# Performance work log

Hardware: AMD Instinct MI355X
Metric: run time of the kernel (lower is better)

Reference implementation:

```python
import jax, jax.numpy as jnp
import numpy as np

B, N_FRAMES, C, S = 4, 32, 256, 16
D = 512            # attn_dim = min(C*S*S, 512)
NHEADS = 8
TOKEN = C * S * S  # 65536
EPS = 1e-5


def _layer_norm_last(x, g, b):
    mu = x.mean(-1, keepdims=True)
    var = x.var(-1, keepdims=True)
    return (x - mu) * jax.lax.rsqrt(var + EPS) * g + b


def _forward(feat, Wp, bp, Wu, bu, Wq, bq, Wk, bk, Wv, bv, Wo, bo, ln1_g, ln1_b,
             Wk1, bk1, Wk2, bk2, Wpc, bpc, gn_g, gn_b, Wf1, bf1, Wf2, bf2,
             dn_g, dn_b, num_frames):
    BN, Cc, H, W = feat.shape
    N = num_frames
    Bb = BN // N
    # 1) flatten frames to tokens and project (B, N, token_dim) -> (B, N, D)
    tokens = feat.reshape(Bb, N, Cc * H * W)
    tp = tokens @ Wp.T + bp
    # contextual grouping with clamped indices: K = v_{n-1}, Q = v_n, V = v_{n+1}
    idx = jnp.arange(N)
    v_prev = tp[:, jnp.maximum(idx - 1, 0)]
    v_next = tp[:, jnp.minimum(idx + 1, N - 1)]
    # 2) MHA with seq_len 1 for Q/K/V (degenerate softmax over a single key)
    dh = D // NHEADS
    q = (tp @ Wq.T + bq).reshape(Bb, N, NHEADS, dh)
    k = (v_prev @ Wk.T + bk).reshape(Bb, N, NHEADS, dh)
    v = (v_next @ Wv.T + bv).reshape(Bb, N, NHEADS, dh)
    scores = jnp.sum(q * k, axis=-1, keepdims=True) / jnp.sqrt(jnp.float32(dh))  # (B,N,h,1)
    wts = jax.nn.softmax(scores, axis=-1)  # identically 1.0 (single key)
    attn = (wts * v).reshape(Bb, N, D) @ Wo.T + bo
    enh = _layer_norm_last(attn + tp, ln1_g, ln1_b)
    # 3) unproject back to feature maps
    feat_attn = (enh @ Wu.T + bu).reshape(BN, Cc, H, W)
    # 4) DynamicConv: per-sample depthwise 3x3 kernels conditioned on GAP
    gap = feat_attn.mean((2, 3))                       # (BN, C)
    hid = jax.nn.relu(gap @ Wk1.T + bk1)
    kern = (hid @ Wk2.T + bk2).reshape(BN, Cc, 3, 3)   # per-sample, per-channel kernels
    xp = jnp.pad(feat_attn, ((0, 0), (0, 0), (1, 1), (1, 1)))
    out = jnp.zeros_like(feat_attn)
    for di in range(3):  # fixed 3x3 kernel taps
        for dj in range(3):
            out = out + kern[:, :, di, dj][:, :, None, None] * xp[:, :, di:di + H, dj:dj + W]
    # 1x1 proj conv
    out = jnp.einsum('nchw,dc->ndhw', out, Wpc) + bpc[:, None, None]
    # GroupNorm(min(32,C))
    G = min(32, Cc)
    og = out.reshape(BN, G, -1)
    mu = og.mean(-1, keepdims=True)
    var = og.var(-1, keepdims=True)
    out = ((og - mu) * jax.lax.rsqrt(var + EPS)).reshape(BN, Cc, H, W)
    feat_dc = out * gn_g[:, None, None] + gn_b[:, None, None]
    # 5) dc_fc (1x1 conv -> relu -> 1x1 conv) + residual, then LayerNorm([C,S,S])
    y = jax.nn.relu(jnp.einsum('nchw,dc->ndhw', feat_dc, Wf1) + bf1[:, None, None])
    y = jnp.einsum('nchw,dc->ndhw', y, Wf2) + bf2[:, None, None]
    z = y + feat_attn
    zf = z.reshape(BN, -1)
    mu = zf.mean(-1, keepdims=True)
    var = zf.var(-1, keepdims=True)
    zn = ((zf - mu) * jax.lax.rsqrt(var + EPS)).reshape(BN, Cc, H, W)
    return zn * dn_g + dn_b


def setup_inputs() -> dict:
    key = jax.random.key(0)
    ks = jax.random.split(key, 16)
    sc = 0.02
    inp = {
        'feat': jax.random.normal(ks[0], (B * N_FRAMES, C, S, S), jnp.float32),
        'Wp': jax.random.normal(ks[1], (D, TOKEN), jnp.float32) * sc,
        'bp': jnp.zeros((D,), jnp.float32),
        'Wu': jax.random.normal(ks[2], (TOKEN, D), jnp.float32) * sc,
        'bu': jnp.zeros((TOKEN,), jnp.float32),
        'Wq': jax.random.normal(ks[3], (D, D), jnp.float32) * sc,
        'bq': jnp.zeros((D,), jnp.float32),
        'Wk': jax.random.normal(ks[4], (D, D), jnp.float32) * sc,
        'bk': jnp.zeros((D,), jnp.float32),
        'Wv': jax.random.normal(ks[5], (D, D), jnp.float32) * sc,
        'bv': jnp.zeros((D,), jnp.float32),
        'Wo': jax.random.normal(ks[6], (D, D), jnp.float32) * sc,
        'bo': jnp.zeros((D,), jnp.float32),
        'ln1_g': jnp.ones((D,), jnp.float32),
        'ln1_b': jnp.zeros((D,), jnp.float32),
        'Wk1': jax.random.normal(ks[7], (C, C), jnp.float32) * sc,
        'bk1': jnp.zeros((C,), jnp.float32),
        'Wk2': jax.random.normal(ks[8], (C * 9, C), jnp.float32) * sc,
        'bk2': jnp.zeros((C * 9,), jnp.float32),
        'Wpc': jax.random.normal(ks[9], (C, C), jnp.float32) * sc,
        'bpc': jnp.zeros((C,), jnp.float32),
        'gn_g': jnp.ones((C,), jnp.float32),
        'gn_b': jnp.zeros((C,), jnp.float32),
        'Wf1': jax.random.normal(ks[10], (C, C), jnp.float32) * sc,
        'bf1': jnp.zeros((C,), jnp.float32),
        'Wf2': jax.random.normal(ks[11], (C, C), jnp.float32) * sc,
        'bf2': jnp.zeros((C,), jnp.float32),
        'dn_g': jnp.ones((C, S, S), jnp.float32),
        'dn_b': jnp.zeros((C, S, S), jnp.float32),
        'num_frames': N_FRAMES,
    }
    return inp


def reference(feat, Wp, bp, Wu, bu, Wq, bq, Wk, bk, Wv, bv, Wo, bo, ln1_g, ln1_b,
              Wk1, bk1, Wk2, bk2, Wpc, bpc, gn_g, gn_b, Wf1, bf1, Wf2, bf2,
              dn_g, dn_b, num_frames):
    return _forward(feat, Wp, bp, Wu, bu, Wq, bq, Wk, bk, Wv, bv, Wo, bo,
                    ln1_g, ln1_b, Wk1, bk1, Wk2, bk2, Wpc, bpc, gn_g, gn_b,
                    Wf1, bf1, Wf2, bf2, dn_g, dn_b, num_frames)
```

## Files before the change

### kernel.cpp

```cpp
#include <hip/hip_runtime.h>


typedef unsigned short u16;
typedef unsigned int u32;
typedef __attribute__((ext_vector_type(8))) short short8;
typedef __attribute__((ext_vector_type(4))) float floatx4;

__device__ __forceinline__ float b2f(u16 h){ return __uint_as_float(((u32)h)<<16); }
__device__ __forceinline__ u16 f2b(float f){
  u32 u = __float_as_uint(f);
  u = (u + 0x7FFFu + ((u>>16)&1u)) >> 16;
  return (u16)u;
}
__device__ __forceinline__ float blo(u32 w){ return __uint_as_float(w<<16); }
__device__ __forceinline__ float bhi(u32 w){ return __uint_as_float(w & 0xFFFF0000u); }
__device__ __forceinline__ bool probe_f32(const u32* p){ return p[0]==0x3F800000u; }

__device__ __forceinline__ float wred(float v){
  #pragma unroll
  for (int o=32;o>0;o>>=1) v += __shfl_down(v, o, 64);
  return v;
}

__device__ __forceinline__ float dot8(uint4 u, const float* t){
  return t[0]*blo(u.x)+t[1]*bhi(u.x)+t[2]*blo(u.y)+t[3]*bhi(u.y)
       + t[4]*blo(u.z)+t[5]*bhi(u.z)+t[6]*blo(u.w)+t[7]*bhi(u.w);
}

struct SrcTab { const void* p[22]; };

__global__ __launch_bounds__(256) void cvt_k(SrcTab st, const u32* probe, u16* dst){
  constexpr int ns[22]   = {262144,262144,65536,589824,65536,65536,65536,65536,65536,
                            65536,512,512,512,512,512,256,2304,256,256,256,256,256};
  constexpr int offs[22] = {0,262144,524288,589824,1179648,1245184,1310720,1376256,1441792,
                            1507328,1572864,1573376,1573888,1574400,1574912,1575424,1575680,
                            1577984,1578240,1578496,1578752,1579008};
  int t = blockIdx.y;
  int e = (blockIdx.x*256 + threadIdx.x)*4;
  if (e >= ns[t]) return;
  u16* d = dst + offs[t] + e;
  if (probe_f32(probe)){
    float4 v = *(const float4*)((const float*)st.p[t] + e);
    d[0]=f2b(v.x); d[1]=f2b(v.y); d[2]=f2b(v.z); d[3]=f2b(v.w);
  } else {
    *(uint2*)d = *(const uint2*)((const u16*)st.p[t] + e);
  }
}

template<int MODE>
__global__ __launch_bounds__(256) void gemm_k(
    const void* __restrict__ Ap, int lda,
    const void* __restrict__ Bp, int ldb,
    void* __restrict__ Cp, int N, int Ktot, int kchunk,
    const u16* __restrict__ bias,
    const float* __restrict__ gnst,
    const u16* __restrict__ gng, const u16* __restrict__ gnb,
    const u16* __restrict__ fres,
    const u32* __restrict__ probe, int araw, int braw)
{
  __shared__ __align__(16) u16 As[64*72];
  __shared__ __align__(16) u16 Bs[64*72];

  const bool pf32 = probe_f32(probe);
  const bool a32 = araw && pf32, b32 = braw && pf32;

  const int tid = threadIdx.x;
  const int lane = tid & 63, wv = tid >> 6;
  const int mw = wv >> 1, nw = wv & 1;
  const int m0 = blockIdx.x * 64, n0 = blockIdx.y * 64;
  int k0 = 0, kend = Ktot;
  if (MODE == 0) { k0 = blockIdx.z * kchunk; kend = k0 + kchunk; }

  floatx4 zf = {0.f,0.f,0.f,0.f};
  floatx4 acc[2][2];
  acc[0][0]=zf; acc[0][1]=zf; acc[1][0]=zf; acc[1][1]=zf;

  const int ml = lane & 15, q = lane >> 4;
  const int ar0 = (mw*32 + ml)*72 + q*8;
  const int ar1 = ar0 + 16*72;
  const int br0 = (nw*32 + ml)*72 + q*8;
  const int br1 = br0 + 16*72;

  for (int kk = k0; kk < kend; kk += 64){
    __syncthreads();
    #pragma unroll
    for (int i=0;i<2;i++){
      int idx = tid + i*256;
      int row = idx >> 3, colc = idx & 7;
      u16* adst = &As[row*72 + colc*8];
      if (MODE == 3){
        const u16* src = (const u16*)Ap + (size_t)(m0+row)*lda + kk + colc*8;
        uint4 u = *(const uint4*)src;
        int nsamp = (m0+row) >> 8;
        int cbase = kk + colc*8;
        int g = cbase >> 3;
        float mu = gnst[(nsamp*32+g)*2], rs = gnst[(nsamp*32+g)*2+1];
        float f[8] = {blo(u.x),bhi(u.x),blo(u.y),bhi(u.y),blo(u.z),bhi(u.z),blo(u.w),bhi(u.w)};
        #pragma unroll
        for (int j=0;j<8;j++){
          int c = cbase + j;
          adst[j] = f2b((f[j]-mu)*rs*b2f(gng[c]) + b2f(gnb[c]));
        }
      } else if (a32){
        const float* src = (const float*)Ap + (size_t)(m0+row)*lda + kk + colc*8;
        float4 v0 = ((const float4*)src)[0];
        float4 v1 = ((const float4*)src)[1];
        adst[0]=f2b(v0.x); adst[1]=f2b(v0.y); adst[2]=f2b(v0.z); adst[3]=f2b(v0.w);
        adst[4]=f2b(v1.x); adst[5]=f2b(v1.y); adst[6]=f2b(v1.z); adst[7]=f2b(v1.w);
      } else {
        const u16* src = (const u16*)Ap + (size_t)(m0+row)*lda + kk + colc*8;
        *(uint4*)adst = *(const uint4*)src;
      }
      u16* bdst = &Bs[row*72 + colc*8];
      if (b32){
        const float* src = (const float*)Bp + (size_t)(n0+row)*ldb + kk + colc*8;
        float4 v0 = ((const float4*)src)[0];
        float4 v1 = ((const float4*)src)[1];
        bdst[0]=f2b(v0.x); bdst[1]=f2b(v0.y); bdst[2]=f2b(v0.z); bdst[3]=f2b(v0.w);
        bdst[4]=f2b(v1.x); bdst[5]=f2b(v1.y); bdst[6]=f2b(v1.z); bdst[7]=f2b(v1.w);
      } else {
        const u16* src = (const u16*)Bp + (size_t)(n0+row)*ldb + kk + colc*8;
        *(uint4*)bdst = *(const uint4*)src;
      }
    }
    __syncthreads();
    #pragma unroll
    for (int ks2=0; ks2<2; ks2++){
      int ko = ks2*32;
      short8 a0 = *(const short8*)&As[ar0 + ko];
      short8 a1 = *(const short8*)&As[ar1 + ko];
      short8 b0 = *(const short8*)&Bs[br0 + ko];
      short8 b1 = *(const short8*)&Bs[br1 + ko];
      acc[0][0] = __builtin_amdgcn_mfma_f32_16x16x32_bf16(a0, b0, acc[0][0], 0,0,0);
      acc[0][1] = __builtin_amdgcn_mfma_f32_16x16x32_bf16(a0, b1, acc[0][1], 0,0,0);
      acc[1][0] = __builtin_amdgcn_mfma_f32_16x16x32_bf16(a1, b0, acc[1][0], 0,0,0);
      acc[1][1] = __builtin_amdgcn_mfma_f32_16x16x32_bf16(a1, b1, acc[1][1], 0,0,0);
    }
  }

  const int colg = lane & 15, quad = lane >> 4;
  #pragma unroll
  for (int mi=0;mi<2;mi++){
    #pragma unroll
    for (int ni=0;ni<2;ni++){
      #pragma unroll
      for (int r=0;r<4;r++){
        int m = m0 + mw*32 + mi*16 + quad*4 + r;
        int n = n0 + nw*32 + ni*16 + colg;
        float v = acc[mi][ni][r];
        if (MODE==0){
          atomicAdd(&((float*)Cp)[(size_t)m*N + n], v);
        } else if (MODE==1){
          ((u16*)Cp)[(size_t)m*N + n] = f2b(v + b2f(bias[n]));
        } else if (MODE==3){
          ((u16*)Cp)[(size_t)m*N + n] = f2b(fmaxf(v + b2f(bias[n]), 0.f));
        } else if (MODE==4){
          int nsp = m >> 8, s = m & 255;
          ((u16*)Cp)[(size_t)m*N + n] =
              f2b(v + b2f(bias[n]) + b2f(fres[(size_t)nsp*65536 + (size_t)n*256 + s]));
        }
      }
    }
  }
}

__global__ __launch_bounds__(512) void attn_ln_k(
    const float* __restrict__ tp, const u16* __restrict__ Wv, const u16* __restrict__ bv,
    const u16* __restrict__ Wo, const u16* __restrict__ bo, const u16* __restrict__ bp,
    const u16* __restrict__ g, const u16* __restrict__ bln, u16* __restrict__ enh)
{
  __shared__ float tpr[512], tpn[512], vv[512], red[16];
  int r = blockIdx.x; int n = r & 31; int rn = (n==31) ? r : r+1;
  int t = threadIdx.x;
  float bpv = b2f(bp[t]);
  tpr[t] = tp[(size_t)r*512 + t] + bpv;
  tpn[t] = tp[(size_t)rn*512 + t] + bpv;
  __syncthreads();
  {
    const uint4* w4 = (const uint4*)(Wv + (size_t)t*512);
    float acc = b2f(bv[t]);
    #pragma unroll 8
    for (int i=0;i<64;i++) acc += dot8(w4[i], &tpn[i*8]);
    vv[t] = acc;
  }
  __syncthreads();
  float x;
  {
    const uint4* w4 = (const uint4*)(Wo + (size_t)t*512);
    float acc = b2f(bo[t]);
    #pragma unroll 8
    for (int i=0;i<64;i++) acc += dot8(w4[i], &vv[i*8]);
    x = acc + tpr[t];
  }
  float s1 = wred(x), s2 = wred(x*x);
  int lane = t & 63, wid = t >> 6;
  if (lane==0){ red[wid] = s1; red[8+wid] = s2; }
  __syncthreads();
  if (t==0){
    float a=0.f, b=0.f;
    #pragma unroll
    for (int i=0;i<8;i++){ a += red[i]; b += red[8+i]; }
    float mu = a/512.f; float var = b/512.f - mu*mu;
    red[0]=mu; red[1]=rsqrtf(var+1e-5f);
  }
  __syncthreads();
  float mu = red[0], rs = red[1];
  enh[(size_t)r*512 + t] = f2b((x-mu)*rs*b2f(g[t]) + b2f(bln[t]));
}

__global__ __launch_bounds__(256) void gap_k(const u16* __restrict__ fa, float* __restrict__ gapb){
  int wid = threadIdx.x>>6, lane = threadIdx.x&63;
  int pair = blockIdx.x*4 + wid;
  const uint2* p = (const uint2*)(fa + (size_t)pair*256);
  uint2 v = p[lane];
  float s = wred(blo(v.x)+bhi(v.x)+blo(v.y)+bhi(v.y));
  if (lane==0) gapb[pair] = s * (1.0f/256.0f);
}

__global__ __launch_bounds__(256) void hidkern_k(
    const float* __restrict__ gapb, const u16* __restrict__ Wk1, const u16* __restrict__ bk1,
    const u16* __restrict__ Wk2, const u16* __restrict__ bk2, float* __restrict__ kernb)
{
  __shared__ float gl[256], hl[256];
  int nn = blockIdx.x, t = threadIdx.x;
  gl[t] = gapb[(size_t)nn*256 + t];
  __syncthreads();
  {
    const uint4* w4 = (const uint4*)(Wk1 + (size_t)t*256);
    float acc = b2f(bk1[t]);
    #pragma unroll 8
    for (int i=0;i<32;i++) acc += dot8(w4[i], &gl[i*8]);
    hl[t] = fmaxf(acc, 0.f);
  }
  __syncthreads();
  for (int qq=0; qq<9; qq++){
    int e = t*9 + qq;
    const uint4* w4 = (const uint4*)(Wk2 + (size_t)e*256);
    float acc = b2f(bk2[e]);
    #pragma unroll 8
    for (int i=0;i<32;i++) acc += dot8(w4[i], &hl[i*8]);
    kernb[(size_t)nn*2304 + e] = acc;
  }
}

__global__ __launch_bounds__(256) void conv_k(
    const u16* __restrict__ fa, const float* __restrict__ kernb, u16* __restrict__ dwb)
{
  int b = blockIdx.x; int h = b & 15; int nn = b >> 4; int c = threadIdx.x;
  float kv[9];
  #pragma unroll
  for (int qq=0; qq<9; qq++) kv[qq] = kernb[(size_t)nn*2304 + c*9 + qq];
  float rowv[3][18];
  #pragma unroll
  for (int di=0; di<3; di++){
    int hh = h + di - 1;
    if (hh >= 0 && hh < 16){
      const u16* rp = fa + (size_t)nn*65536 + (size_t)c*256 + hh*16;
      rowv[di][0] = 0.f; rowv[di][17] = 0.f;
      #pragma unroll
      for (int w=0; w<16; w++) rowv[di][w+1] = b2f(rp[w]);
    } else {
      #pragma unroll
      for (int x=0; x<18; x++) rowv[di][x] = 0.f;
    }
  }
  #pragma unroll
  for (int w=0; w<16; w++){
    float o = 0.f;
    #pragma unroll
    for (int di=0; di<3; di++)
      o += kv[di*3]*rowv[di][w] + kv[di*3+1]*rowv[di][w+1] + kv[di*3+2]*rowv[di][w+2];
    dwb[((size_t)nn*256 + h*16 + w)*256 + c] = f2b(o);
  }
}

__global__ __launch_bounds__(256) void gnstats_k(const u16* __restrict__ out2, float* __restrict__ gnst){
  int wid = threadIdx.x>>6, lane = threadIdx.x&63;
  int grp = blockIdx.x*4 + wid; int nn = grp >> 5; int gg = grp & 31;
  const u16* base = out2 + (size_t)nn*65536 + gg*8;
  float s=0.f, ss=0.f;
  #pragma unroll 4
  for (int i=0;i<32;i++){
    int f = i*64 + lane; int sidx = f >> 3; int j = f & 7;
    float v = b2f(base[(size_t)sidx*256 + j]);
    s += v; ss += v*v;
  }
  s = wred(s); ss = wred(ss);
  if (lane==0){
    float mu = s/2048.f; float var = ss/2048.f - mu*mu;
    gnst[grp*2] = mu; gnst[grp*2+1] = rsqrtf(var + 1e-5f);
  }
}

__global__ __launch_bounds__(256) void lnstats_k(const u16* __restrict__ z, float* __restrict__ lnst){
  __shared__ float red[8];
  int nn = blockIdx.x, t = threadIdx.x;
  const uint4* p = (const uint4*)(z + (size_t)nn*65536);
  float s=0.f, ss=0.f;
  for (int i=0;i<32;i++){
    uint4 v = p[(size_t)i*256 + t];
    float f0=blo(v.x),f1=bhi(v.x),f2=blo(v.y),f3=bhi(v.y);
    float f4=blo(v.z),f5=bhi(v.z),f6=blo(v.w),f7=bhi(v.w);
    s  += (f0+f1)+(f2+f3)+(f4+f5)+(f6+f7);
    ss += (f0*f0+f1*f1)+(f2*f2+f3*f3)+(f4*f4+f5*f5)+(f6*f6+f7*f7);
  }
  s = wred(s); ss = wred(ss);
  int lane = t&63, wid = t>>6;
  if (lane==0){ red[wid]=s; red[4+wid]=ss; }
  __syncthreads();
  if (t==0){
    float a=red[0]+red[1]+red[2]+red[3];
    float b=red[4]+red[5]+red[6]+red[7];
    float mu = a/65536.f; float var = b/65536.f - mu*mu;
    lnst[nn*2] = mu; lnst[nn*2+1] = rsqrtf(var + 1e-5f);
  }
}

__global__ __launch_bounds__(256) void final_k(
    const u16* __restrict__ z, const float* __restrict__ lnst,
    const u16* __restrict__ dng, const u16* __restrict__ dnb,
    void* __restrict__ outp, const u32* __restrict__ probe)
{
  __shared__ float zt[32*257];
  const bool pf32 = probe_f32(probe);
  int b = blockIdx.x; int nn = b >> 3; int s0 = (b & 7)*32;
  int t = threadIdx.x;
  {
    int srow = t >> 3; int c0 = (t & 7)*32;
    const uint4* p = (const uint4*)(z + (size_t)nn*65536 + (size_t)(s0+srow)*256 + c0);
    float* dst = &zt[srow*257 + c0];
    #pragma unroll
    for (int i=0;i<4;i++){
      uint4 v = p[i];
      dst[i*8+0]=blo(v.x); dst[i*8+1]=bhi(v.x); dst[i*8+2]=blo(v.y); dst[i*8+3]=bhi(v.y);
      dst[i*8+4]=blo(v.z); dst[i*8+5]=bhi(v.z); dst[i*8+6]=blo(v.w); dst[i*8+7]=bhi(v.w);
    }
  }
  __syncthreads();
  float mu = lnst[nn*2], rs = lnst[nn*2+1];
  int sl = t & 31, cq = t >> 5;
  for (int i=0;i<32;i++){
    int c = i*8 + cq;
    float v = (zt[sl*257 + c] - mu) * rs;
    int gidx = c*256 + s0 + sl;
    float res = v*b2f(dng[gidx]) + b2f(dnb[gidx]);
    size_t oi = (size_t)nn*65536 + gidx;
    if (pf32) ((float*)outp)[oi] = res;
    else      ((u16*)outp)[oi]   = f2b(res);
  }
}

extern "C" void kernel_launch(void* const* d_in, const int* in_sizes, int n_in,
                              void* d_out, int out_size, void* d_ws, size_t ws_size,
                              hipStream_t stream) {
  (void)in_sizes; (void)n_in; (void)out_size; (void)ws_size;
  const u32* probe = (const u32*)d_in[21];

  char* w = (char*)d_ws;
  u16* cvt = (u16*)w;
  u16 *cWv  = cvt+0,       *cWo  = cvt+262144, *cWk1 = cvt+524288, *cWk2 = cvt+589824;
  u16 *cWpc = cvt+1179648, *cWf1 = cvt+1245184,*cWf2 = cvt+1310720;
  u16 *cdng = cvt+1376256, *cdnb = cvt+1441792,*cbu  = cvt+1507328;
  u16 *cbp  = cvt+1572864, *cbv  = cvt+1573376,*cbo  = cvt+1573888;
  u16 *cln1g= cvt+1574400, *cln1b= cvt+1574912,*cbk1 = cvt+1575424,*cbk2 = cvt+1575680;
  u16 *cbpc = cvt+1577984, *cgng = cvt+1578240,*cgnb = cvt+1578496;
  u16 *cbf1 = cvt+1578752, *cbf2 = cvt+1579008;

  float* tp_raw = (float*)(w + 4194304);
  u16*   enh    = (u16*)  (w + 4456448);
  float* gapb   = (float*)(w + 4587520);
  float* kernb  = (float*)(w + 4718592);
  float* gnst   = (float*)(w + 5898240);
  float* lnst   = (float*)(w + 5931008);
  u16*   fa     = (u16*)  (w + 8388608);
  u16*   out2   = (u16*)  (w + 25165824);
  u16*   z      = out2;
  u16*   dwb    = (u16*)d_out;
  u16*   y1     = dwb;

  SrcTab st;
  st.p[0]=d_in[9];  st.p[1]=d_in[11]; st.p[2]=d_in[15]; st.p[3]=d_in[17];
  st.p[4]=d_in[19]; st.p[5]=d_in[23]; st.p[6]=d_in[25]; st.p[7]=d_in[27];
  st.p[8]=d_in[28]; st.p[9]=d_in[4];  st.p[10]=d_in[2]; st.p[11]=d_in[10];
  st.p[12]=d_in[12];st.p[13]=d_in[13];st.p[14]=d_in[14];st.p[15]=d_in[16];
  st.p[16]=d_in[18];st.p[17]=d_in[20];st.p[18]=d_in[21];st.p[19]=d_in[22];
  st.p[20]=d_in[24];st.p[21]=d_in[26];

  cvt_k<<<dim3(576,22), 256, 0, stream>>>(st, probe, cvt);
  hipMemsetAsync(tp_raw, 0, 128*512*4, stream);
  gemm_k<0><<<dim3(2,8,128), 256, 0, stream>>>(d_in[0], 65536, d_in[1], 65536, tp_raw,
      512, 65536, 512, nullptr, nullptr, nullptr, nullptr, nullptr, probe, 1, 1);
  attn_ln_k<<<128, 512, 0, stream>>>(tp_raw, cWv, cbv, cWo, cbo, cbp, cln1g, cln1b, enh);
  gemm_k<1><<<dim3(2,1024,1), 256, 0, stream>>>(enh, 512, d_in[3], 512, fa,
      65536, 512, 0, cbu, nullptr, nullptr, nullptr, nullptr, probe, 0, 1);
  gap_k<<<8192, 256, 0, stream>>>(fa, gapb);
  hidkern_k<<<128, 256, 0, stream>>>(gapb, cWk1, cbk1, cWk2, cbk2, kernb);
  conv_k<<<2048, 256, 0, stream>>>(fa, kernb, dwb);
  gemm_k<1><<<dim3(512,4,1), 256, 0, stream>>>(dwb, 256, cWpc, 256, out2,
      256, 256, 0, cbpc, nullptr, nullptr, nullptr, nullptr, probe, 0, 0);
  gnstats_k<<<1024, 256, 0, stream>>>(out2, gnst);
  gemm_k<3><<<dim3(512,4,1), 256, 0, stream>>>(out2, 256, cWf1, 256, y1,
      256, 256, 0, cbf1, gnst, cgng, cgnb, nullptr, probe, 0, 0);
  gemm_k<4><<<dim3(512,4,1), 256, 0, stream>>>(y1, 256, cWf2, 256, z,
      256, 256, 0, cbf2, nullptr, nullptr, nullptr, fa, probe, 0, 0);
  lnstats_k<<<128, 256, 0, stream>>>(z, lnst);
  final_k<<<1024, 256, 0, stream>>>(z, lnst, cdng, cdnb, d_out, probe);
}
```

Measured before the change: 644.8 us.

## Register-prefetch next GEMM tile to overlap global loads with MFMA

Restructures the GEMM main loop into a two-stage software pipeline. The next K-tile is loaded into registers while the current tile is staged into LDS and consumed by MFMA, and the loop is unrolled by two with ping-pong register buffers. __syncthreads is replaced with raw s_barrier plus an explicit lgkmcnt wait, and the per-element LDS stores become vectorized 16-byte stores. The goal is to hide global memory latency, at the cost of more registers. The loop now steps by 128 and always processes kk+64, so it assumes the K range is a multiple of 128. The bare barriers also depend on correct ordering of LDS writes.

```diff
diff --git a/kernel.cpp b/kernel.cpp
--- a/kernel.cpp
+++ b/kernel.cpp
@@ -25,6 +25,18 @@
 __device__ __forceinline__ float dot8(uint4 u, const float* t){
   return t[0]*blo(u.x)+t[1]*bhi(u.x)+t[2]*blo(u.y)+t[3]*bhi(u.y)
        + t[4]*blo(u.z)+t[5]*bhi(u.z)+t[6]*blo(u.w)+t[7]*bhi(u.w);
+}
+
+__device__ __forceinline__ void bar_lgkm(){
+  asm volatile("s_waitcnt lgkmcnt(0)" ::: "memory");
+  __builtin_amdgcn_sched_barrier(0);
+  __builtin_amdgcn_s_barrier();
+  asm volatile("" ::: "memory");
+}
+__device__ __forceinline__ void bar(){
+  asm volatile("" ::: "memory");
+  __builtin_amdgcn_s_barrier();
+  asm volatile("" ::: "memory");
 }
 
 struct SrcTab { const void* p[22]; };
@@ -81,49 +93,77 @@
   const int br0 = (nw*32 + ml)*72 + q*8;
   const int br1 = br0 + 16*72;
 
-  for (int kk = k0; kk < kend; kk += 64){
-    __syncthreads();
+  const int row0 = tid >> 3, colc = tid & 7;
+
+  auto ld_tiles = [&](uint4 (&pa)[2][2], uint4 (&pb)[2][2], int kk){
     #pragma unroll
     for (int i=0;i<2;i++){
-      int idx = tid + i*256;
-      int row = idx >> 3, colc = idx & 7;
+      int row = row0 + i*32;
+      if (a32){
+        const float* s = (const float*)Ap + (size_t)(m0+row)*lda + kk + colc*8;
+        pa[i][0] = ((const uint4*)s)[0];
+        pa[i][1] = ((const uint4*)s)[1];
+      } else {
+        const u16* s = (const u16*)Ap + (size_t)(m0+row)*lda + kk + colc*8;
+        pa[i][0] = *(const uint4*)s;
+      }
+      if (b32){
+        const float* s = (const float*)Bp + (size_t)(n0+row)*ldb + kk + colc*8;
+        pb[i][0] = ((const uint4*)s)[0];
+        pb[i][1] = ((const uint4*)s)[1];
+      } else {
+        const u16* s = (const u16*)Bp + (size_t)(n0+row)*ldb + kk + colc*8;
+        pb[i][0] = *(const uint4*)s;
+      }
+    }
+  };
+
+  auto stage = [&](uint4 (&pa)[2][2], uint4 (&pb)[2][2], int kk){
+    #pragma unroll
+    for (int i=0;i<2;i++){
+      int row = row0 + i*32;
       u16* adst = &As[row*72 + colc*8];
       if (MODE == 3){
-        const u16* src = (const u16*)Ap + (size_t)(m0+row)*lda + kk + colc*8;
-        uint4 u = *(const uint4*)src;
+        uint4 u = pa[i][0];
         int nsamp = (m0+row) >> 8;
         int cbase = kk + colc*8;
         int g = cbase >> 3;
         float mu = gnst[(nsamp*32+g)*2], rs = gnst[(nsamp*32+g)*2+1];
         float f[8] = {blo(u.x),bhi(u.x),blo(u.y),bhi(u.y),blo(u.z),bhi(u.z),blo(u.w),bhi(u.w)};
+        u16 tmp[8];
         #pragma unroll
         for (int j=0;j<8;j++){
           int c = cbase + j;
-          adst[j] = f2b((f[j]-mu)*rs*b2f(gng[c]) + b2f(gnb[c]));
+          tmp[j] = f2b((f[j]-mu)*rs*b2f(gng[c]) + b2f(gnb[c]));
         }
+        *(uint4*)adst = *(uint4*)tmp;
       } else if (a32){
-        const float* src = (const float*)Ap + (size_t)(m0+row)*lda + kk + colc*8;
-        float4 v0 = ((const float4*)src)[0];
-        float4 v1 = ((const float4*)src)[1];
-        adst[0]=f2b(v0.x); adst[1]=f2b(v0.y); adst[2]=f2b(v0.z); adst[3]=f2b(v0.w);
-        adst[4]=f2b(v1.x); adst[5]=f2b(v1.y); adst[6]=f2b(v1.z); adst[7]=f2b(v1.w);
+        uint4 v0 = pa[i][0], v1 = pa[i][1];
+        u16 tmp[8];
+        tmp[0]=f2b(__uint_as_float(v0.x)); tmp[1]=f2b(__uint_as_float(v0.y));
+        tmp[2]=f2b(__uint_as_float(v0.z)); tmp[3]=f2b(__uint_as_float(v0.w));
+        tmp[4]=f2b(__uint_as_float(v1.x)); tmp[5]=f2b(__uint_as_float(v1.y));
+        tmp[6]=f2b(__uint_as_float(v1.z)); tmp[7]=f2b(__uint_as_float(v1.w));
+        *(uint4*)adst = *(uint4*)tmp;
       } else {
-        const u16* src = (const u16*)Ap + (size_t)(m0+row)*lda + kk + colc*8;
-        *(uint4*)adst = *(const uint4*)src;
+        *(uint4*)adst = pa[i][0];
       }
       u16* bdst = &Bs[row*72 + colc*8];
       if (b32){
-        const float* src = (const float*)Bp + (size_t)(n0+row)*ldb + kk + colc*8;
-        float4 v0 = ((const float4*)src)[0];
-        float4 v1 = ((const float4*)src)[1];
-        bdst[0]=f2b(v0.x); bdst[1]=f2b(v0.y); bdst[2]=f2b(v0.z); bdst[3]=f2b(v0.w);
-        bdst[4]=f2b(v1.x); bdst[5]=f2b(v1.y); bdst[6]=f2b(v1.z); bdst[7]=f2b(v1.w);
+        uint4 v0 = pb[i][0], v1 = pb[i][1];
+        u16 tmp[8];
+        tmp[0]=f2b(__uint_as_float(v0.x)); tmp[1]=f2b(__uint_as_float(v0.y));
+        tmp[2]=f2b(__uint_as_float(v0.z)); tmp[3]=f2b(__uint_as_float(v0.w));
+        tmp[4]=f2b(__uint_as_float(v1.x)); tmp[5]=f2b(__uint_as_float(v1.y));
+        tmp[6]=f2b(__uint_as_float(v1.z)); tmp[7]=f2b(__uint_as_float(v1.w));
+        *(uint4*)bdst = *(uint4*)tmp;
       } else {
-        const u16* src = (const u16*)Bp + (size_t)(n0+row)*ldb + kk + colc*8;
-        *(uint4*)bdst = *(const uint4*)src;
+        *(uint4*)bdst = pb[i][0];
       }
     }
-    __syncthreads();
+  };
+
+  auto mfma_step = [&](){
     #pragma unroll
     for (int ks2=0; ks2<2; ks2++){
       int ko = ks2*32;
@@ -136,6 +176,21 @@
       acc[1][0] = __builtin_amdgcn_mfma_f32_16x16x32_bf16(a1, b0, acc[1][0], 0,0,0);
       acc[1][1] = __builtin_amdgcn_mfma_f32_16x16x32_bf16(a1, b1, acc[1][1], 0,0,0);
     }
+  };
+
+  uint4 pa0[2][2], pb0[2][2], pa1[2][2], pb1[2][2];
+  ld_tiles(pa0, pb0, k0);
+  for (int kk = k0; kk < kend; kk += 128){
+    bar();
+    ld_tiles(pa1, pb1, kk + 64);
+    stage(pa0, pb0, kk);
+    bar_lgkm();
+    mfma_step();
+    bar();
+    if (kk + 128 < kend) ld_tiles(pa0, pb0, kk + 128);
+    stage(pa1, pb1, kk + 64);
+    bar_lgkm();
+    mfma_step();
   }
 
   const int colg = lane & 15, quad = lane >> 4;
```

Result: faster. 616.4 us (-4.4%).
